# Kernel optimization log

Hardware: AMD Instinct MI355X
Metric: run time of the kernel (lower is better)

## Reference

```python
import jax, jax.numpy as jnp
import numpy as np

N, E = 50000, 800000          # nodes, edges
F_IN, H, C = 32, 64, 7        # input feats, hidden, classes
EPS = 1e-5                    # BatchNorm eps


def setup_inputs() -> dict:
    key = jax.random.key(0)
    ks = jax.random.split(key, 16)
    inp = {
        "x": jax.random.normal(ks[0], (N, F_IN), jnp.float32),
        "edge_index": jax.random.randint(ks[1], (2, E), 0, N),
        "edge_attr": jax.random.uniform(ks[2], (E, 1), jnp.float32),
    }

    def conv_params(k, cin, cout, i):
        k1, k2 = jax.random.split(k)
        s = 1.0 / np.sqrt(cin)
        inp[f"W{i}"] = jax.random.uniform(k1, (2, cin, cout), jnp.float32, -s, s)  # spline kernel weights
        inp[f"R{i}"] = jax.random.uniform(k2, (cin, cout), jnp.float32, -s, s)     # root weight
        inp[f"B{i}"] = jnp.zeros((cout,), jnp.float32)

    conv_params(ks[3], F_IN, H, 0)
    conv_params(ks[4], H, H, 1)
    conv_params(ks[5], H, C, 2)
    for i in range(2):  # BatchNorm (eval mode: running stats)
        inp[f"G{i}"] = jnp.ones((H,), jnp.float32)
        inp[f"BE{i}"] = jnp.zeros((H,), jnp.float32)
        inp[f"RM{i}"] = 0.1 * jax.random.normal(ks[6 + 2 * i], (H,), jnp.float32)
        inp[f"RV{i}"] = jax.random.uniform(ks[7 + 2 * i], (H,), jnp.float32, 0.5, 1.5)
    return inp


def spline_conv(x, src, dst, u, W, R, B):
    # dim=1, kernel_size=2, degree=1 open B-spline:
    # basis = (1-u, u) with weight indices (0, 1) for u in [0,1).
    basis = jnp.stack([1.0 - u, u], axis=1)               # [E, 2]
    msg = jnp.einsum('ec,ek,kco->eo', x[src], basis, W)    # gather + basis-weighted linear
    agg = jax.ops.segment_sum(msg, dst, num_segments=N)    # scatter-add
    deg = jax.ops.segment_sum(jnp.ones((src.shape[0],), x.dtype), dst, num_segments=N)
    agg = agg / jnp.maximum(deg, 1.0)[:, None]             # aggr='mean' (default)
    return agg + x @ R + B                                 # root weight + bias


def batch_norm(x, g, b, rm, rv):
    return (x - rm) * jax.lax.rsqrt(rv + EPS) * g + b


def reference(x, edge_index, edge_attr,
              W0, R0, B0, W1, R1, B1, W2, R2, B2,
              G0, BE0, RM0, RV0, G1, BE1, RM1, RV1):
    src, dst = edge_index[0], edge_index[1]
    u = edge_attr[:, 0]
    h = spline_conv(x, src, dst, u, W0, R0, B0)
    h = jax.nn.elu(batch_norm(h, G0, BE0, RM0, RV0))
    h = spline_conv(h, src, dst, u, W1, R1, B1)
    h = jax.nn.elu(batch_norm(h, G1, BE1, RM1, RV1))
    h = spline_conv(h, src, dst, u, W2, R2, B2)
    return jax.nn.log_softmax(h, axis=1)
```

## Files before the change

kernel.cpp:

```cpp
#include <hip/hip_runtime.h>
#include <hip/hip_fp16.h>
#include <math.h>

#define NN 50000
#define NE 800000
#define EPSV 1e-5f
#define BSHIFT 7
#define BSIZE 128
#define NB 391
#define CAP 3840

typedef _Float16 h2f   __attribute__((ext_vector_type(2)));
typedef _Float16 f16x8 __attribute__((ext_vector_type(8)));
typedef float    f32x4 __attribute__((ext_vector_type(4)));

__global__ __launch_bounds__(64) void prep_all_kernel(
        const float* __restrict__ W0, const float* __restrict__ R0,
        const float* __restrict__ W1, const float* __restrict__ R1,
        const float* __restrict__ W2, const float* __restrict__ R2,
        const float* __restrict__ B0, const float* __restrict__ B1,
        const float* __restrict__ G0, const float* __restrict__ BE0,
        const float* __restrict__ RM0, const float* __restrict__ RV0,
        const float* __restrict__ G1, const float* __restrict__ BE1,
        const float* __restrict__ RM1, const float* __restrict__ RV1,
        __half* __restrict__ Bf0, __half* __restrict__ Bf1, __half* __restrict__ Bf7,
        float* __restrict__ bn0, float* __restrict__ bn1,
        int* __restrict__ bcursor) {
    int lane = threadIdx.x;
    int bid = blockIdx.x;
    int c = lane & 15;
    int kbase = ((lane >> 4) << 3);
    _Float16 vals[8];
    if (bid < 12) {
        int ks = bid >> 2, nt = bid & 3;
        int n = nt * 16 + c;
#pragma unroll
        for (int j = 0; j < 8; ++j) {
            int kg = ks * 32 + kbase + j;
            float v = (kg < 64) ? W0[(kg & 1) * 2048 + (kg >> 1) * 64 + n]
                                : R0[(kg - 64) * 64 + n];
            vals[j] = (_Float16)v;
        }
        *reinterpret_cast<f16x8*>(Bf0 + ((size_t)(bid * 64 + lane)) * 8) =
            *reinterpret_cast<f16x8*>(vals);
    } else if (bid < 36) {
        int t = bid - 12;
        int ks = t >> 2, nt = t & 3;
        int n = nt * 16 + c;
#pragma unroll
        for (int j = 0; j < 8; ++j) {
            int kg = ks * 32 + kbase + j;
            float v = (kg < 128) ? W1[(kg & 1) * 4096 + (kg >> 1) * 64 + n]
                                 : R1[(kg - 128) * 64 + n];
            vals[j] = (_Float16)v;
        }
        *reinterpret_cast<f16x8*>(Bf1 + ((size_t)(t * 64 + lane)) * 8) =
            *reinterpret_cast<f16x8*>(vals);
    } else if (bid < 40) {
        int ksnt = bid - 36;
        int ks = ksnt >> 1, nt = ksnt & 1;
#pragma unroll
        for (int j = 0; j < 8; ++j) {
            int k = ks * 32 + kbase + j;
            float v = 0.f;
            if (nt == 0) {
                if (c < 7)                 v = W2[k * 7 + c];
                else if (c >= 8 && c < 15) v = W2[448 + k * 7 + (c - 8)];
            } else {
                if (c < 7)                 v = R2[k * 7 + c];
            }
            vals[j] = (_Float16)v;
        }
        *reinterpret_cast<f16x8*>(Bf7 + ((size_t)(ksnt * 64 + lane)) * 8) =
            *reinterpret_cast<f16x8*>(vals);
    } else if (bid == 40) {
        float s = G0[lane] * rsqrtf(RV0[lane] + EPSV);
        bn0[lane] = s;
        bn0[64 + lane] = B0[lane] * s + BE0[lane] - RM0[lane] * s;
    } else if (bid == 41) {
        float s = G1[lane] * rsqrtf(RV1[lane] + EPSV);
        bn1[lane] = s;
        bn1[64 + lane] = B1[lane] * s + BE1[lane] - RM1[lane] * s;
    } else {
        int b = (bid - 42) * 64 + lane;
        if (b < NB) bcursor[b] = b * CAP;
    }
}

__global__ __launch_bounds__(256) void binB_xh_kernel(
        const int* __restrict__ src, const int* __restrict__ dst,
        const float* __restrict__ attr, int* __restrict__ bcursor,
        uint2* __restrict__ es1, int E,
        const float* __restrict__ x, __half* __restrict__ xh) {
    __shared__ int hist[NB];
    __shared__ int base[NB];
    if (blockIdx.x >= NB) {
        int t = (blockIdx.x - NB) * 256 + threadIdx.x;
        size_t idx = (size_t)t * 8;
        if (idx < (size_t)NN * 32) {
            float4 f0 = *reinterpret_cast<const float4*>(x + idx);
            float4 f1 = *reinterpret_cast<const float4*>(x + idx + 4);
            _Float16 v[8] = {(_Float16)f0.x, (_Float16)f0.y, (_Float16)f0.z, (_Float16)f0.w,
                             (_Float16)f1.x, (_Float16)f1.y, (_Float16)f1.z, (_Float16)f1.w};
            *reinterpret_cast<f16x8*>(xh + idx) = *reinterpret_cast<f16x8*>(v);
        }
        return;
    }
    for (int i = threadIdx.x; i < NB; i += blockDim.x) hist[i] = 0;
    __syncthreads();
    const int chunk = (E + NB - 1) / NB;
    int e0 = blockIdx.x * chunk;
    int e1 = e0 + chunk; if (e1 > E) e1 = E;
    unsigned su[8]; unsigned char dlv[8]; short bv[8];
#pragma unroll
    for (int j = 0; j < 8; ++j) {
        int e = e0 + threadIdx.x + j * 256;
        if (e < e1) {
            int d = dst[e];
            int b = d >> BSHIFT;
            __half uh = __float2half_rn(attr[e]);
            su[j]  = ((unsigned)src[e] << 16) | (unsigned)__half_as_ushort(uh);
            dlv[j] = (unsigned char)(d & (BSIZE - 1));
            bv[j]  = (short)b;
            atomicAdd(&hist[b], 1);
        }
    }
    __syncthreads();
    for (int i = threadIdx.x; i < NB; i += blockDim.x) {
        int cnt = hist[i];
        base[i] = cnt ? atomicAdd(&bcursor[i], cnt) : 0;
        hist[i] = 0;
    }
    __syncthreads();
#pragma unroll
    for (int j = 0; j < 8; ++j) {
        int e = e0 + threadIdx.x + j * 256;
        if (e < e1) {
            int b = bv[j];
            int slot = base[b] + atomicAdd(&hist[b], 1);
            uint2 rec; rec.x = su[j]; rec.y = (unsigned)dlv[j];
            es1[slot] = rec;
        }
    }
}

__global__ __launch_bounds__(256) void placeC_kernel(const int* __restrict__ bcursor,
                                                     const uint2* __restrict__ es1,
                                                     int2* __restrict__ rowrange,
                                                     uint2* __restrict__ es8) {
    __shared__ int hist[BSIZE];
    __shared__ int stmp[BSIZE];
    __shared__ int cur[BSIZE];
    int b = blockIdx.x;
    int t = threadIdx.x;
    int bs = b * CAP;
    int be = bcursor[b];
    if (t < BSIZE) hist[t] = 0;
    __syncthreads();
    unsigned su[10]; unsigned char dlv[10];
#pragma unroll
    for (int j = 0; j < 10; ++j) {
        int i = bs + t + j * 256;
        if (i < be) {
            uint2 r = es1[i];
            su[j]  = r.x;
            dlv[j] = (unsigned char)r.y;
            atomicAdd(&hist[dlv[j]], 1);
        }
    }
    __syncthreads();
    if (t < BSIZE) {
        int v = hist[t];
        int pv = (v + 15) & ~15;
        int incl = pv;
#pragma unroll
        for (int o = 1; o < 64; o <<= 1) {
            int nv = __shfl_up(incl, o, 64);
            if ((t & 63) >= o) incl += nv;
        }
        stmp[t] = incl;
    }
    __syncthreads();
    if (t < BSIZE) {
        int v = hist[t];
        int pv = (v + 15) & ~15;
        int excl = stmp[t] - pv + ((t >= 64) ? stmp[63] : 0);
        cur[t] = excl;
        int node = b * BSIZE + t;
        if (node < NN) {
            int2 rr; rr.x = bs + excl; rr.y = (v << 16) | pv;
            rowrange[node] = rr;
        }
    }
    __syncthreads();
#pragma unroll
    for (int j = 0; j < 10; ++j) {
        int i = bs + t + j * 256;
        if (i < be) {
            unsigned r = su[j];
            int dl = dlv[j];
            int slot = bs + atomicAdd(&cur[dl], 1);
            __half uh = __ushort_as_half((unsigned short)(r & 0xffffu));
            __half2 p = __halves2half2(__hsub(__ushort_as_half((unsigned short)0x3C00u), uh), uh);
            uint2 rec;
            rec.x = r >> 16;
            rec.y = *reinterpret_cast<unsigned*>(&p);
            es8[slot] = rec;
        }
    }
    __syncthreads();
    if (t < BSIZE) {
        int v = hist[t];
        int pv = (v + 15) & ~15;
        int start = bs + cur[t];
        int endp  = bs + (cur[t] - v) + pv;
        uint2 z; z.x = 0u; z.y = 0u;
        for (int k = start; k < endp; ++k) es8[k] = z;
    }
}

__global__ __launch_bounds__(256, 8) void gf0_kernel(const int2* __restrict__ rowrange,
                                                     const uint2* __restrict__ es8,
                                                     const __half* __restrict__ xh,
                                                     const __half* __restrict__ Bf0,
                                                     const float* __restrict__ bn,
                                                     __half* __restrict__ h0, int n_nodes) {
    __shared__ __align__(16) char ldsS[16 * 128];
    const int lane = threadIdx.x & 63;
    const int wid  = threadIdx.x >> 6;
    const int nb = blockIdx.x * 16;
    const unsigned c2 = (unsigned)((lane & 31) << 1);
    const char* xb = (const char*)xh;
    int2 rr4 = rowrange[nb + wid * 4 + (lane & 3)];
#pragma unroll 1
    for (int k = 0; k < 4; ++k) {
        int row = wid * 4 + k;
        int beg  = __builtin_amdgcn_readfirstlane(__shfl(rr4.x, k, 64));
        int meta = __builtin_amdgcn_readfirstlane(__shfl(rr4.y, k, 64));
        int end = beg + (meta & 0xffff);
        float a0 = 0.f, a1 = 0.f, a2 = 0.f, a3 = 0.f;
        float a4 = 0.f, a5 = 0.f, a6 = 0.f, a7 = 0.f;
        float b0 = 0.f, b1 = 0.f, b2 = 0.f, b3 = 0.f;
        float b4 = 0.f, b5 = 0.f, b6 = 0.f, b7 = 0.f;
        int i = beg + (lane >> 5);
        for (; i + 14 < end; i += 16) {
            uint2 q0 = es8[i];
            uint2 q1 = es8[i + 2];
            uint2 q2 = es8[i + 4];
            uint2 q3 = es8[i + 6];
            uint2 q4 = es8[i + 8];
            uint2 q5 = es8[i + 10];
            uint2 q6 = es8[i + 12];
            uint2 q7 = es8[i + 14];
            __half x0 = *(const __half*)(xb + ((q0.x << 6) | c2));
            __half x1 = *(const __half*)(xb + ((q1.x << 6) | c2));
            __half x2 = *(const __half*)(xb + ((q2.x << 6) | c2));
            __half x3 = *(const __half*)(xb + ((q3.x << 6) | c2));
            __half x4 = *(const __half*)(xb + ((q4.x << 6) | c2));
            __half x5 = *(const __half*)(xb + ((q5.x << 6) | c2));
            __half x6 = *(const __half*)(xb + ((q6.x << 6) | c2));
            __half x7 = *(const __half*)(xb + ((q7.x << 6) | c2));
            __half2 u0 = __builtin_bit_cast(__half2, q0.y);
            __half2 u1 = __builtin_bit_cast(__half2, q1.y);
            __half2 u2 = __builtin_bit_cast(__half2, q2.y);
            __half2 u3 = __builtin_bit_cast(__half2, q3.y);
            __half2 u4 = __builtin_bit_cast(__half2, q4.y);
            __half2 u5 = __builtin_bit_cast(__half2, q5.y);
            __half2 u6 = __builtin_bit_cast(__half2, q6.y);
            __half2 u7 = __builtin_bit_cast(__half2, q7.y);
            float f0 = __half2float(x0), f1 = __half2float(x1);
            float f2 = __half2float(x2), f3 = __half2float(x3);
            float f4 = __half2float(x4), f5 = __half2float(x5);
            float f6 = __half2float(x6), f7 = __half2float(x7);
            a0 = fmaf(__low2float(u0), f0, a0); b0 = fmaf(__high2float(u0), f0, b0);
            a1 = fmaf(__low2float(u1), f1, a1); b1 = fmaf(__high2float(u1), f1, b1);
            a2 = fmaf(__low2float(u2), f2, a2); b2 = fmaf(__high2float(u2), f2, b2);
            a3 = fmaf(__low2float(u3), f3, a3); b3 = fmaf(__high2float(u3), f3, b3);
            a4 = fmaf(__low2float(u4), f4, a4); b4 = fmaf(__high2float(u4), f4, b4);
            a5 = fmaf(__low2float(u5), f5, a5); b5 = fmaf(__high2float(u5), f5, b5);
            a6 = fmaf(__low2float(u6), f6, a6); b6 = fmaf(__high2float(u6), f6, b6);
            a7 = fmaf(__low2float(u7), f7, a7); b7 = fmaf(__high2float(u7), f7, b7);
        }
        float a = ((a0 + a1) + (a2 + a3)) + ((a4 + a5) + (a6 + a7));
        float b = ((b0 + b1) + (b2 + b3)) + ((b4 + b5) + (b6 + b7));
        a += __shfl_xor(a, 32);
        b += __shfl_xor(b, 32);
        float degv = (float)(meta >> 16);
        if (degv < 1.f) degv = 1.f;
        float inv = 1.f / degv;
        if (lane < 32) {
            int byte = (row * 128 + (lane & 31) * 4) ^ ((row & 7) << 4);
            *reinterpret_cast<__half2*>(ldsS + byte) = __floats2half2_rn(a * inv, b * inv);
        }
    }
    __syncthreads();
    if (wid != 0) return;

    const int m0 = nb;
    f32x4 acc[4];
#pragma unroll
    for (int i = 0; i < 4; ++i) acc[i] = (f32x4){0.f, 0.f, 0.f, 0.f};
    const int rowl = lane & 15;
    const int g = lane >> 4;
    const int koff = g << 3;
    const int swz = (rowl & 7) << 4;
    const f16x8* bf = reinterpret_cast<const f16x8*>(Bf0);
    f16x8 a0v = *reinterpret_cast<const f16x8*>(ldsS + ((rowl * 128 + g * 16) ^ swz));
    f16x8 a1v = *reinterpret_cast<const f16x8*>(ldsS + ((rowl * 128 + 64 + g * 16) ^ swz));
    f16x8 a2v = *reinterpret_cast<const f16x8*>((const _Float16*)xh + (size_t)(m0 + rowl) * 32 + koff);
#pragma unroll
    for (int nt = 0; nt < 4; ++nt)
        acc[nt] = __builtin_amdgcn_mfma_f32_16x16x32_f16(a0v, bf[nt * 64 + lane], acc[nt], 0, 0, 0);
#pragma unroll
    for (int nt = 0; nt < 4; ++nt)
        acc[nt] = __builtin_amdgcn_mfma_f32_16x16x32_f16(a1v, bf[(4 + nt) * 64 + lane], acc[nt], 0, 0, 0);
#pragma unroll
    for (int nt = 0; nt < 4; ++nt)
        acc[nt] = __builtin_amdgcn_mfma_f32_16x16x32_f16(a2v, bf[(8 + nt) * 64 + lane], acc[nt], 0, 0, 0);
    const int c_lo  = lane & 15;
    const int rbase = ((lane >> 4) << 2);
#pragma unroll
    for (int nt = 0; nt < 4; ++nt) {
        int cc = nt * 16 + c_lo;
        float sc = bn[cc], sh = bn[64 + cc];
#pragma unroll
        for (int r = 0; r < 4; ++r) {
            int rw = m0 + rbase + r;
            float v = acc[nt][r] * sc + sh;
            v = v > 0.f ? v : expm1f(v);
            h0[(size_t)rw * 64 + cc] = __float2half(v);
        }
    }
}

__global__ __launch_bounds__(256, 8) void gf1_kernel(const int2* __restrict__ rowrange,
                                                     const uint2* __restrict__ es8,
                                                     const __half* __restrict__ h0,
                                                     const __half* __restrict__ Bf1,
                                                     const __half* __restrict__ Bf7,
                                                     const float* __restrict__ bn,
                                                     const float* __restrict__ Bb2,
                                                     __half* __restrict__ Yab7H,
                                                     float* __restrict__ Z7,
                                                     int n_nodes) {
    __shared__ __align__(16) char ldsS[16 * 256];
    __shared__ __align__(16) char ldsH[16 * 128];
    const int lane = threadIdx.x & 63;
    const int wid  = threadIdx.x >> 6;
    const int nb = blockIdx.x * 16;
    const unsigned c2 = (unsigned)(lane << 1);
    const char* xb = (const char*)h0;
    int2 rr4 = rowrange[nb + wid * 4 + (lane & 3)];
#pragma unroll 1
    for (int k = 0; k < 4; ++k) {
        int row = wid * 4 + k;
        int beg  = __builtin_amdgcn_readfirstlane(__shfl(rr4.x, k, 64));
        int meta = __builtin_amdgcn_readfirstlane(__shfl(rr4.y, k, 64));
        int end = beg + (meta & 0xffff);
        float a0 = 0.f, a1 = 0.f, a2 = 0.f, a3 = 0.f;
        float a4 = 0.f, a5 = 0.f, a6 = 0.f, a7 = 0.f;
        float b0 = 0.f, b1 = 0.f, b2 = 0.f, b3 = 0.f;
        float b4 = 0.f, b5 = 0.f, b6 = 0.f, b7 = 0.f;
        for (int i = beg; i + 15 < end; i += 16) {
            uint4 p0 = *reinterpret_cast<const uint4*>(es8 + i);
            uint4 p1 = *reinterpret_cast<const uint4*>(es8 + i + 2);
            uint4 p2 = *reinterpret_cast<const uint4*>(es8 + i + 4);
            uint4 p3 = *reinterpret_cast<const uint4*>(es8 + i + 6);
            uint4 p4 = *reinterpret_cast<const uint4*>(es8 + i + 8);
            uint4 p5 = *reinterpret_cast<const uint4*>(es8 + i + 10);
            uint4 p6 = *reinterpret_cast<const uint4*>(es8 + i + 12);
            uint4 p7 = *reinterpret_cast<const uint4*>(es8 + i + 14);
            __half x0 = *(const __half*)(xb + ((p0.x << 7) | c2));
            __half x1 = *(const __half*)(xb + ((p0.z << 7) | c2));
            __half x2 = *(const __half*)(xb + ((p1.x << 7) | c2));
            __half x3 = *(const __half*)(xb + ((p1.z << 7) | c2));
            __half x4 = *(const __half*)(xb + ((p2.x << 7) | c2));
            __half x5 = *(const __half*)(xb + ((p2.z << 7) | c2));
            __half x6 = *(const __half*)(xb + ((p3.x << 7) | c2));
            __half x7 = *(const __half*)(xb + ((p3.z << 7) | c2));
            __half x8 = *(const __half*)(xb + ((p4.x << 7) | c2));
            __half x9 = *(const __half*)(xb + ((p4.z << 7) | c2));
            __half xa = *(const __half*)(xb + ((p5.x << 7) | c2));
            __half xc = *(const __half*)(xb + ((p5.z << 7) | c2));
            __half xd = *(const __half*)(xb + ((p6.x << 7) | c2));
            __half xe = *(const __half*)(xb + ((p6.z << 7) | c2));
            __half xf = *(const __half*)(xb + ((p7.x << 7) | c2));
            __half xg = *(const __half*)(xb + ((p7.z << 7) | c2));
            __half2 u0 = __builtin_bit_cast(__half2, p0.y);
            __half2 u1 = __builtin_bit_cast(__half2, p0.w);
            __half2 u2 = __builtin_bit_cast(__half2, p1.y);
            __half2 u3 = __builtin_bit_cast(__half2, p1.w);
            __half2 u4 = __builtin_bit_cast(__half2, p2.y);
            __half2 u5 = __builtin_bit_cast(__half2, p2.w);
            __half2 u6 = __builtin_bit_cast(__half2, p3.y);
            __half2 u7 = __builtin_bit_cast(__half2, p3.w);
            __half2 u8 = __builtin_bit_cast(__half2, p4.y);
            __half2 u9 = __builtin_bit_cast(__half2, p4.w);
            __half2 ua = __builtin_bit_cast(__half2, p5.y);
            __half2 uc = __builtin_bit_cast(__half2, p5.w);
            __half2 ud = __builtin_bit_cast(__half2, p6.y);
            __half2 ue = __builtin_bit_cast(__half2, p6.w);
            __half2 uf = __builtin_bit_cast(__half2, p7.y);
            __half2 ug = __builtin_bit_cast(__half2, p7.w);
            float f0 = __half2float(x0), f1 = __half2float(x1);
            float f2 = __half2float(x2), f3 = __half2float(x3);
            float f4 = __half2float(x4), f5 = __half2float(x5);
            float f6 = __half2float(x6), f7 = __half2float(x7);
            float f8 = __half2float(x8), f9 = __half2float(x9);
            float fa = __half2float(xa), fc = __half2float(xc);
            float fd = __half2float(xd), fe = __half2float(xe);
            float ff = __half2float(xf), fg = __half2float(xg);
            a0 = fmaf(__low2float(u0), f0, a0); b0 = fmaf(__high2float(u0), f0, b0);
            a1 = fmaf(__low2float(u1), f1, a1); b1 = fmaf(__high2float(u1), f1, b1);
            a2 = fmaf(__low2float(u2), f2, a2); b2 = fmaf(__high2float(u2), f2, b2);
            a3 = fmaf(__low2float(u3), f3, a3); b3 = fmaf(__high2float(u3), f3, b3);
            a4 = fmaf(__low2float(u4), f4, a4); b4 = fmaf(__high2float(u4), f4, b4);
            a5 = fmaf(__low2float(u5), f5, a5); b5 = fmaf(__high2float(u5), f5, b5);
            a6 = fmaf(__low2float(u6), f6, a6); b6 = fmaf(__high2float(u6), f6, b6);
            a7 = fmaf(__low2float(u7), f7, a7); b7 = fmaf(__high2float(u7), f7, b7);
            a0 = fmaf(__low2float(u8), f8, a0); b0 = fmaf(__high2float(u8), f8, b0);
            a1 = fmaf(__low2float(u9), f9, a1); b1 = fmaf(__high2float(u9), f9, b1);
            a2 = fmaf(__low2float(ua), fa, a2); b2 = fmaf(__high2float(ua), fa, b2);
            a3 = fmaf(__low2float(uc), fc, a3); b3 = fmaf(__high2float(uc), fc, b3);
            a4 = fmaf(__low2float(ud), fd, a4); b4 = fmaf(__high2float(ud), fd, b4);
            a5 = fmaf(__low2float(ue), fe, a5); b5 = fmaf(__high2float(ue), fe, b5);
            a6 = fmaf(__low2float(uf), ff, a6); b6 = fmaf(__high2float(uf), ff, b6);
            a7 = fmaf(__low2float(ug), fg, a7); b7 = fmaf(__high2float(ug), fg, b7);
        }
        float a = ((a0 + a1) + (a2 + a3)) + ((a4 + a5) + (a6 + a7));
        float b = ((b0 + b1) + (b2 + b3)) + ((b4 + b5) + (b6 + b7));
        float degv = (float)(meta >> 16);
        if (degv < 1.f) degv = 1.f;
        float inv = 1.f / degv;
        int byte = (row * 256 + lane * 4) ^ ((row & 7) << 4);
        *reinterpret_cast<__half2*>(ldsS + byte) = __floats2half2_rn(a * inv, b * inv);
    }
    __syncthreads();
    if (wid != 0) return;

    const int m0 = nb;
    f32x4 acc[4];
#pragma unroll
    for (int i = 0; i < 4; ++i) acc[i] = (f32x4){0.f, 0.f, 0.f, 0.f};
    const int rowl = lane & 15;
    const int g = lane >> 4;
    const int koff = g << 3;
    const int swz = (rowl & 7) << 4;
    const f16x8* bf = reinterpret_cast<const f16x8*>(Bf1);
    const _Float16* hp = (const _Float16*)h0 + (size_t)(m0 + rowl) * 64 + koff;
#pragma unroll
    for (int ks = 0; ks < 6; ++ks) {
        f16x8 av;
        if (ks < 4) av = *reinterpret_cast<const f16x8*>(ldsS + ((rowl * 256 + ks * 64 + g * 16) ^ swz));
        else        av = *reinterpret_cast<const f16x8*>(hp + (ks - 4) * 32);
#pragma unroll
        for (int nt = 0; nt < 4; ++nt)
            acc[nt] = __builtin_amdgcn_mfma_f32_16x16x32_f16(av, bf[(ks * 4 + nt) * 64 + lane], acc[nt], 0, 0, 0);
    }
    const int c_lo  = lane & 15;
    const int rbase = ((lane >> 4) << 2);
#pragma unroll
    for (int nt = 0; nt < 4; ++nt) {
        int cc = nt * 16 + c_lo;
        float sc = bn[cc], sh = bn[64 + cc];
#pragma unroll
        for (int r = 0; r < 4; ++r) {
            float v = acc[nt][r] * sc + sh;
            v = v > 0.f ? v : expm1f(v);
            int rl = rbase + r;
            *reinterpret_cast<__half*>(ldsH + ((rl * 128 + cc * 2) ^ ((rl & 7) << 4))) = __float2half(v);
        }
    }

    f32x4 acc7[2];
    acc7[0] = (f32x4){0.f, 0.f, 0.f, 0.f};
    acc7[1] = (f32x4){0.f, 0.f, 0.f, 0.f};
    const f16x8* bf7 = reinterpret_cast<const f16x8*>(Bf7);
#pragma unroll
    for (int ks = 0; ks < 2; ++ks) {
        f16x8 av = *reinterpret_cast<const f16x8*>(ldsH + ((rowl * 128 + ks * 64 + g * 16) ^ swz));
#pragma unroll
        for (int nt = 0; nt < 2; ++nt)
            acc7[nt] = __builtin_amdgcn_mfma_f32_16x16x32_f16(av, bf7[(ks * 2 + nt) * 64 + lane], acc7[nt], 0, 0, 0);
    }
#pragma unroll
    for (int r = 0; r < 4; ++r) {
        int rw = m0 + rbase + r;
        if (c_lo < 7) {
            Yab7H[((size_t)rw << 4) + 2 * c_lo] = __float2half(acc7[0][r]);
            Z7[((size_t)rw << 3) + c_lo] = acc7[1][r] + Bb2[c_lo];
        } else if (c_lo >= 8 && c_lo < 15) {
            Yab7H[((size_t)rw << 4) + 2 * (c_lo - 8) + 1] = __float2half(acc7[0][r]);
        }
    }
}

__global__ void gather7_final_kernel(const int2* __restrict__ rowrange,
                                     const uint2* __restrict__ es8,
                                     const __half2* __restrict__ Yab7H,
                                     const float* __restrict__ Z7,
                                     float* __restrict__ out, int n_nodes) {
    int t = blockIdx.x * blockDim.x + threadIdx.x;
    int n = t >> 3;
    int c = t & 7;
    if (n >= n_nodes) return;
    int2 rr = rowrange[n];
    int beg = rr.x;
    int end = beg + (rr.y & 0xffff);
    const unsigned c4 = (unsigned)(c << 2);
    const char* yb = (const char*)Yab7H;
    float acc0 = 0.f, acc1 = 0.f, acc2 = 0.f, acc3 = 0.f;
    if (c < 7) {
        for (int i = beg; i + 7 < end; i += 8) {
            uint2 q0 = es8[i];
            uint2 q1 = es8[i + 1];
            uint2 q2 = es8[i + 2];
            uint2 q3 = es8[i + 3];
            uint2 q4 = es8[i + 4];
            uint2 q5 = es8[i + 5];
            uint2 q6 = es8[i + 6];
            uint2 q7 = es8[i + 7];
            __half2 v0 = *(const __half2*)(yb + ((q0.x << 5) | c4));
            __half2 v1 = *(const __half2*)(yb + ((q1.x << 5) | c4));
            __half2 v2 = *(const __half2*)(yb + ((q2.x << 5) | c4));
            __half2 v3 = *(const __half2*)(yb + ((q3.x << 5) | c4));
            __half2 v4 = *(const __half2*)(yb + ((q4.x << 5) | c4));
            __half2 v5 = *(const __half2*)(yb + ((q5.x << 5) | c4));
            __half2 v6 = *(const __half2*)(yb + ((q6.x << 5) | c4));
            __half2 v7 = *(const __half2*)(yb + ((q7.x << 5) | c4));
            acc0 = __builtin_amdgcn_fdot2(__builtin_bit_cast(h2f, v0), __builtin_bit_cast(h2f, q0.y), acc0, false);
            acc1 = __builtin_amdgcn_fdot2(__builtin_bit_cast(h2f, v1), __builtin_bit_cast(h2f, q1.y), acc1, false);
            acc2 = __builtin_amdgcn_fdot2(__builtin_bit_cast(h2f, v2), __builtin_bit_cast(h2f, q2.y), acc2, false);
            acc3 = __builtin_amdgcn_fdot2(__builtin_bit_cast(h2f, v3), __builtin_bit_cast(h2f, q3.y), acc3, false);
            acc0 = __builtin_amdgcn_fdot2(__builtin_bit_cast(h2f, v4), __builtin_bit_cast(h2f, q4.y), acc0, false);
            acc1 = __builtin_amdgcn_fdot2(__builtin_bit_cast(h2f, v5), __builtin_bit_cast(h2f, q5.y), acc1, false);
            acc2 = __builtin_amdgcn_fdot2(__builtin_bit_cast(h2f, v6), __builtin_bit_cast(h2f, q6.y), acc2, false);
            acc3 = __builtin_amdgcn_fdot2(__builtin_bit_cast(h2f, v7), __builtin_bit_cast(h2f, q7.y), acc3, false);
        }
    }
    float acc = (acc0 + acc1) + (acc2 + acc3);
    float degv = (float)(rr.y >> 16);
    if (degv < 1.f) degv = 1.f;
    float v = (c < 7) ? (acc / degv + Z7[(n << 3) + c]) : -1e30f;
    float m = v;
#pragma unroll
    for (int o = 1; o < 8; o <<= 1) m = fmaxf(m, __shfl_xor(m, o, 8));
    float ex = (c < 7) ? expf(v - m) : 0.f;
    float ssum = ex;
#pragma unroll
    for (int o = 1; o < 8; o <<= 1) ssum += __shfl_xor(ssum, o, 8);
    if (c < 7) out[n * 7 + c] = v - m - logf(ssum);
}

extern "C" void kernel_launch(void* const* d_in, const int* in_sizes, int n_in,
                              void* d_out, int out_size, void* d_ws, size_t ws_size,
                              hipStream_t stream) {
    const float* x    = (const float*)d_in[0];
    const int*   ei   = (const int*)d_in[1];
    const float* attr = (const float*)d_in[2];
    const float* W0 = (const float*)d_in[3];
    const float* R0 = (const float*)d_in[4];
    const float* B0 = (const float*)d_in[5];
    const float* W1 = (const float*)d_in[6];
    const float* R1 = (const float*)d_in[7];
    const float* B1 = (const float*)d_in[8];
    const float* W2 = (const float*)d_in[9];
    const float* R2 = (const float*)d_in[10];
    const float* B2 = (const float*)d_in[11];
    const float* G0  = (const float*)d_in[12];
    const float* BE0 = (const float*)d_in[13];
    const float* RM0 = (const float*)d_in[14];
    const float* RV0 = (const float*)d_in[15];
    const float* G1  = (const float*)d_in[16];
    const float* BE1 = (const float*)d_in[17];
    const float* RM1 = (const float*)d_in[18];
    const float* RV1 = (const float*)d_in[19];

    const int* src = ei;
    const int* dst = ei + NE;
    float* out = (float*)d_out;

    char* ws = (char*)d_ws;
    size_t off = 0;
    auto alloc = [&](size_t bytes) { char* p = ws + off; off += (bytes + 255) & ~size_t(255); return p; };
    int*    bcursor  = (int*)    alloc(NB * sizeof(int));
    int2*   rowrange = (int2*)   alloc((size_t)NN * sizeof(int2));
    uint2*  es1      = (uint2*)  alloc((size_t)NB * CAP * sizeof(uint2));
    uint2*  es8      = (uint2*)  alloc((size_t)NB * CAP * sizeof(uint2));
    __half* Bf0      = (__half*) alloc((size_t)12 * 64 * 8 * sizeof(__half));
    __half* Bf1      = (__half*) alloc((size_t)24 * 64 * 8 * sizeof(__half));
    __half* Bf7      = (__half*) alloc((size_t)4 * 64 * 8 * sizeof(__half));
    float*  bn0      = (float*)  alloc(128 * sizeof(float));
    float*  bn1      = (float*)  alloc(128 * sizeof(float));
    __half* xh       = (__half*) alloc((size_t)(NN + 64) * 32 * sizeof(__half));
    __half* h0       = (__half*) alloc((size_t)(NN + 64) * 64 * sizeof(__half));
    __half* Yab7H    = (__half*) alloc((size_t)NN * 16 * sizeof(__half));
    float*  Z7       = (float*)  alloc((size_t)NN * 8 * sizeof(float));

    const int B = 256;
    const int gF    = (NN + 15) / 16;
    const int gN8   = (NN * 8 + B - 1) / B;
    const int gConv = ((NN * 32 / 8) + B - 1) / B;
    const int gPrep = 42 + (NB + 63) / 64;

    prep_all_kernel<<<gPrep, 64, 0, stream>>>(W0, R0, W1, R1, W2, R2, B0, B1,
                                              G0, BE0, RM0, RV0, G1, BE1, RM1, RV1,
                                              Bf0, Bf1, Bf7, bn0, bn1, bcursor);

    binB_xh_kernel<<<NB + gConv, B, 0, stream>>>(src, dst, attr, bcursor, es1, NE, x, xh);

    placeC_kernel<<<NB, B, 0, stream>>>(bcursor, es1, rowrange, es8);

    gf0_kernel<<<gF, B, 0, stream>>>(rowrange, es8, xh, Bf0, bn0, h0, NN);

    gf1_kernel<<<gF, B, 0, stream>>>(rowrange, es8, h0, Bf1, Bf7, bn1, B2, Yab7H, Z7, NN);

    gather7_final_kernel<<<gN8, B, 0, stream>>>(rowrange, es8, (const __half2*)Yab7H, Z7, out, NN);
}
```

Before: 192.6 us.

## Widen binning blocks to 1024 threads and split MFMA tiles across all waves

The binning and placement kernels now launch 1024-thread blocks, so each thread holds fewer edges in registers and per-bin work is spread over more waves. In the two fused gather+GEMM kernels, the post-aggregation MFMA work was done by wave 0 alone. It is now split so each of the four waves computes one 16-column output tile, and two waves share the final 7-class projection after an extra barrier. This removes the serial single-wave GEMM tail at the cost of an added __syncthreads and larger blocks that may reduce occupancy flexibility.

```diff
diff --git a/kernel.cpp b/kernel.cpp
--- a/kernel.cpp
+++ b/kernel.cpp
@@ -87,7 +87,7 @@
     }
 }
 
-__global__ __launch_bounds__(256) void binB_xh_kernel(
+__global__ __launch_bounds__(1024) void binB_xh_kernel(
         const int* __restrict__ src, const int* __restrict__ dst,
         const float* __restrict__ attr, int* __restrict__ bcursor,
         uint2* __restrict__ es1, int E,
@@ -95,7 +95,7 @@
     __shared__ int hist[NB];
     __shared__ int base[NB];
     if (blockIdx.x >= NB) {
-        int t = (blockIdx.x - NB) * 256 + threadIdx.x;
+        int t = (blockIdx.x - NB) * 1024 + threadIdx.x;
         size_t idx = (size_t)t * 8;
         if (idx < (size_t)NN * 32) {
             float4 f0 = *reinterpret_cast<const float4*>(x + idx);
@@ -111,10 +111,10 @@
     const int chunk = (E + NB - 1) / NB;
     int e0 = blockIdx.x * chunk;
     int e1 = e0 + chunk; if (e1 > E) e1 = E;
-    unsigned su[8]; unsigned char dlv[8]; short bv[8];
-#pragma unroll
-    for (int j = 0; j < 8; ++j) {
-        int e = e0 + threadIdx.x + j * 256;
+    unsigned su[2]; unsigned char dlv[2]; short bv[2];
+#pragma unroll
+    for (int j = 0; j < 2; ++j) {
+        int e = e0 + threadIdx.x + j * 1024;
         if (e < e1) {
             int d = dst[e];
             int b = d >> BSHIFT;
@@ -133,8 +133,8 @@
     }
     __syncthreads();
 #pragma unroll
-    for (int j = 0; j < 8; ++j) {
-        int e = e0 + threadIdx.x + j * 256;
+    for (int j = 0; j < 2; ++j) {
+        int e = e0 + threadIdx.x + j * 1024;
         if (e < e1) {
             int b = bv[j];
             int slot = base[b] + atomicAdd(&hist[b], 1);
@@ -144,10 +144,10 @@
     }
 }
 
-__global__ __launch_bounds__(256) void placeC_kernel(const int* __restrict__ bcursor,
-                                                     const uint2* __restrict__ es1,
-                                                     int2* __restrict__ rowrange,
-                                                     uint2* __restrict__ es8) {
+__global__ __launch_bounds__(1024) void placeC_kernel(const int* __restrict__ bcursor,
+                                                      const uint2* __restrict__ es1,
+                                                      int2* __restrict__ rowrange,
+                                                      uint2* __restrict__ es8) {
     __shared__ int hist[BSIZE];
     __shared__ int stmp[BSIZE];
     __shared__ int cur[BSIZE];
@@ -157,10 +157,10 @@
     int be = bcursor[b];
     if (t < BSIZE) hist[t] = 0;
     __syncthreads();
-    unsigned su[10]; unsigned char dlv[10];
-#pragma unroll
-    for (int j = 0; j < 10; ++j) {
-        int i = bs + t + j * 256;
+    unsigned su[3]; unsigned char dlv[3];
+#pragma unroll
+    for (int j = 0; j < 3; ++j) {
+        int i = bs + t + j * 1024;
         if (i < be) {
             uint2 r = es1[i];
             su[j]  = r.x;
@@ -194,8 +194,8 @@
     }
     __syncthreads();
 #pragma unroll
-    for (int j = 0; j < 10; ++j) {
-        int i = bs + t + j * 256;
+    for (int j = 0; j < 3; ++j) {
+        int i = bs + t + j * 1024;
         if (i < be) {
             unsigned r = su[j];
             int dl = dlv[j];
@@ -294,12 +294,9 @@
         }
     }
     __syncthreads();
-    if (wid != 0) return;
 
     const int m0 = nb;
-    f32x4 acc[4];
-#pragma unroll
-    for (int i = 0; i < 4; ++i) acc[i] = (f32x4){0.f, 0.f, 0.f, 0.f};
+    f32x4 acc = (f32x4){0.f, 0.f, 0.f, 0.f};
     const int rowl = lane & 15;
     const int g = lane >> 4;
     const int koff = g << 3;
@@ -308,25 +305,18 @@
     f16x8 a0v = *reinterpret_cast<const f16x8*>(ldsS + ((rowl * 128 + g * 16) ^ swz));
     f16x8 a1v = *reinterpret_cast<const f16x8*>(ldsS + ((rowl * 128 + 64 + g * 16) ^ swz));
     f16x8 a2v = *reinterpret_cast<const f16x8*>((const _Float16*)xh + (size_t)(m0 + rowl) * 32 + koff);
-#pragma unroll
-    for (int nt = 0; nt < 4; ++nt)
-        acc[nt] = __builtin_amdgcn_mfma_f32_16x16x32_f16(a0v, bf[nt * 64 + lane], acc[nt], 0, 0, 0);
-#pragma unroll
-    for (int nt = 0; nt < 4; ++nt)
-        acc[nt] = __builtin_amdgcn_mfma_f32_16x16x32_f16(a1v, bf[(4 + nt) * 64 + lane], acc[nt], 0, 0, 0);
-#pragma unroll
-    for (int nt = 0; nt < 4; ++nt)
-        acc[nt] = __builtin_amdgcn_mfma_f32_16x16x32_f16(a2v, bf[(8 + nt) * 64 + lane], acc[nt], 0, 0, 0);
+    acc = __builtin_amdgcn_mfma_f32_16x16x32_f16(a0v, bf[wid * 64 + lane], acc, 0, 0, 0);
+    acc = __builtin_amdgcn_mfma_f32_16x16x32_f16(a1v, bf[(4 + wid) * 64 + lane], acc, 0, 0, 0);
+    acc = __builtin_amdgcn_mfma_f32_16x16x32_f16(a2v, bf[(8 + wid) * 64 + lane], acc, 0, 0, 0);
     const int c_lo  = lane & 15;
     const int rbase = ((lane >> 4) << 2);
-#pragma unroll
-    for (int nt = 0; nt < 4; ++nt) {
-        int cc = nt * 16 + c_lo;
+    {
+        int cc = wid * 16 + c_lo;
         float sc = bn[cc], sh = bn[64 + cc];
 #pragma unroll
         for (int r = 0; r < 4; ++r) {
             int rw = m0 + rbase + r;
-            float v = acc[nt][r] * sc + sh;
+            float v = acc[r] * sc + sh;
             v = v > 0.f ? v : expm1f(v);
             h0[(size_t)rw * 64 + cc] = __float2half(v);
         }
@@ -436,12 +426,9 @@
         *reinterpret_cast<__half2*>(ldsS + byte) = __floats2half2_rn(a * inv, b * inv);
     }
     __syncthreads();
-    if (wid != 0) return;
 
     const int m0 = nb;
-    f32x4 acc[4];
-#pragma unroll
-    for (int i = 0; i < 4; ++i) acc[i] = (f32x4){0.f, 0.f, 0.f, 0.f};
+    f32x4 acc = (f32x4){0.f, 0.f, 0.f, 0.f};
     const int rowl = lane & 15;
     const int g = lane >> 4;
     const int koff = g << 3;
@@ -453,44 +440,48 @@
         f16x8 av;
         if (ks < 4) av = *reinterpret_cast<const f16x8*>(ldsS + ((rowl * 256 + ks * 64 + g * 16) ^ swz));
         else        av = *reinterpret_cast<const f16x8*>(hp + (ks - 4) * 32);
-#pragma unroll
-        for (int nt = 0; nt < 4; ++nt)
-            acc[nt] = __builtin_amdgcn_mfma_f32_16x16x32_f16(av, bf[(ks * 4 + nt) * 64 + lane], acc[nt], 0, 0, 0);
+        acc = __builtin_amdgcn_mfma_f32_16x16x32_f16(av, bf[(ks * 4 + wid) * 64 + lane], acc, 0, 0, 0);
     }
     const int c_lo  = lane & 15;
     const int rbase = ((lane >> 4) << 2);
-#pragma unroll
-    for (int nt = 0; nt < 4; ++nt) {
-        int cc = nt * 16 + c_lo;
+    {
+        int cc = wid * 16 + c_lo;
         float sc = bn[cc], sh = bn[64 + cc];
 #pragma unroll
         for (int r = 0; r < 4; ++r) {
-            float v = acc[nt][r] * sc + sh;
+            float v = acc[r] * sc + sh;
             v = v > 0.f ? v : expm1f(v);
             int rl = rbase + r;
             *reinterpret_cast<__half*>(ldsH + ((rl * 128 + cc * 2) ^ ((rl & 7) << 4))) = __float2half(v);
         }
     }
-
-    f32x4 acc7[2];
-    acc7[0] = (f32x4){0.f, 0.f, 0.f, 0.f};
-    acc7[1] = (f32x4){0.f, 0.f, 0.f, 0.f};
+    __syncthreads();
+    if (wid >= 2) return;
+
+    f32x4 acc7 = (f32x4){0.f, 0.f, 0.f, 0.f};
     const f16x8* bf7 = reinterpret_cast<const f16x8*>(Bf7);
 #pragma unroll
     for (int ks = 0; ks < 2; ++ks) {
         f16x8 av = *reinterpret_cast<const f16x8*>(ldsH + ((rowl * 128 + ks * 64 + g * 16) ^ swz));
-#pragma unroll
-        for (int nt = 0; nt < 2; ++nt)
-            acc7[nt] = __builtin_amdgcn_mfma_f32_16x16x32_f16(av, bf7[(ks * 2 + nt) * 64 + lane], acc7[nt], 0, 0, 0);
-    }
-#pragma unroll
-    for (int r = 0; r < 4; ++r) {
-        int rw = m0 + rbase + r;
-        if (c_lo < 7) {
-            Yab7H[((size_t)rw << 4) + 2 * c_lo] = __float2half(acc7[0][r]);
-            Z7[((size_t)rw << 3) + c_lo] = acc7[1][r] + Bb2[c_lo];
-        } else if (c_lo >= 8 && c_lo < 15) {
-            Yab7H[((size_t)rw << 4) + 2 * (c_lo - 8) + 1] = __float2half(acc7[0][r]);
+        acc7 = __builtin_amdgcn_mfma_f32_16x16x32_f16(av, bf7[(ks * 2 + wid) * 64 + lane], acc7, 0, 0, 0);
+    }
+    if (wid == 0) {
+#pragma unroll
+        for (int r = 0; r < 4; ++r) {
+            int rw = m0 + rbase + r;
+            if (c_lo < 7) {
+                Yab7H[((size_t)rw << 4) + 2 * c_lo] = __float2half(acc7[r]);
+            } else if (c_lo >= 8 && c_lo < 15) {
+                Yab7H[((size_t)rw << 4) + 2 * (c_lo - 8) + 1] = __float2half(acc7[r]);
+            }
+        }
+    } else {
+#pragma unroll
+        for (int r = 0; r < 4; ++r) {
+            int rw = m0 + rbase + r;
+            if (c_lo < 7) {
+                Z7[((size_t)rw << 3) + c_lo] = acc7[r] + Bb2[c_lo];
+            }
         }
     }
 }
@@ -598,18 +589,19 @@
     float*  Z7       = (float*)  alloc((size_t)NN * 8 * sizeof(float));
 
     const int B = 256;
+    const int B4w = 1024;
     const int gF    = (NN + 15) / 16;
     const int gN8   = (NN * 8 + B - 1) / B;
-    const int gConv = ((NN * 32 / 8) + B - 1) / B;
+    const int gConv = ((NN * 32) + (B4w * 8) - 1) / (B4w * 8);
     const int gPrep = 42 + (NB + 63) / 64;
 
     prep_all_kernel<<<gPrep, 64, 0, stream>>>(W0, R0, W1, R1, W2, R2, B0, B1,
                                               G0, BE0, RM0, RV0, G1, BE1, RM1, RV1,
                                               Bf0, Bf1, Bf7, bn0, bn1, bcursor);
 
-    binB_xh_kernel<<<NB + gConv, B, 0, stream>>>(src, dst, attr, bcursor, es1, NE, x, xh);
-
-    placeC_kernel<<<NB, B, 0, stream>>>(bcursor, es1, rowrange, es8);
+    binB_xh_kernel<<<NB + gConv, B4w, 0, stream>>>(src, dst, attr, bcursor, es1, NE, x, xh);
+
+    placeC_kernel<<<NB, B4w, 0, stream>>>(bcursor, es1, rowrange, es8);
 
     gf0_kernel<<<gF, B, 0, stream>>>(rowrange, es8, xh, Bf0, bn0, h0, NN);
 
```

Result: no change. 189.0 us (-1.9%).
